# Optimization experiments

Measured on AMD Instinct MI355X. Metric: run time of the kernel, lower is better.

Reference implementation:

```python
import jax, jax.numpy as jnp
import numpy as np

D_MODEL = 1024
NUM_HEADS = 16
DEPTH = D_MODEL // NUM_HEADS  # 64
B, S = 4, 2048
NEG_BIG = -1000000000.0


def setup_inputs() -> dict:
    key = jax.random.key(0)
    ks = jax.random.split(key, 9)
    # Glorot-uniform per-head projection weights, stacked over heads: [H, d_model, depth]
    lim_qkv = np.sqrt(6.0 / (D_MODEL + DEPTH)).astype(np.float32)
    lim_o = np.sqrt(6.0 / (D_MODEL + D_MODEL)).astype(np.float32)
    x = jax.random.normal(ks[0], (B, S, D_MODEL), dtype=jnp.float32)
    attention_mask = jnp.ones((B, S, 1), dtype=jnp.float32)
    Wq = jax.random.uniform(ks[1], (NUM_HEADS, D_MODEL, DEPTH), jnp.float32, -lim_qkv, lim_qkv)
    Wk = jax.random.uniform(ks[2], (NUM_HEADS, D_MODEL, DEPTH), jnp.float32, -lim_qkv, lim_qkv)
    Wv = jax.random.uniform(ks[3], (NUM_HEADS, D_MODEL, DEPTH), jnp.float32, -lim_qkv, lim_qkv)
    bq = jnp.zeros((NUM_HEADS, DEPTH), jnp.float32)
    bk = jnp.zeros((NUM_HEADS, DEPTH), jnp.float32)
    bv = jnp.zeros((NUM_HEADS, DEPTH), jnp.float32)
    Wo = jax.random.uniform(ks[4], (D_MODEL, D_MODEL), jnp.float32, -lim_o, lim_o)
    bo = jnp.zeros((D_MODEL,), jnp.float32)
    return {"x": x, "attention_mask": attention_mask, "Wq": Wq, "bq": bq,
            "Wk": Wk, "bk": bk, "Wv": Wv, "bv": bv, "Wo": Wo, "bo": bo}


def reference(x, attention_mask, Wq, bq, Wk, bk, Wv, bv, Wo, bo):
    # Batched over heads (same math as the per-head Python loop + concat).
    # x: [B,S,D]; Wq/Wk/Wv: [H,D,depth]; bq/bk/bv: [H,depth]
    q = jnp.einsum('bsd,hde->bhse', x, Wq) + bq[None, :, None, :]
    k = jnp.einsum('bsd,hde->bhse', x, Wk) + bk[None, :, None, :]
    v = jnp.einsum('bsd,hde->bhse', x, Wv) + bv[None, :, None, :]
    scale = 1.0 / jnp.sqrt(jnp.asarray(DEPTH, dtype=x.dtype))
    scores = jnp.einsum('bhse,bhte->bhst', q, k) * scale  # [B,H,S,S]
    # original: mask.transpose(-2,-1) -> [B,1,S], broadcast over query rows; add head axis
    mask_t = jnp.swapaxes(attention_mask, -2, -1)[:, None]  # [B,1,1,S]
    scores = scores + (1.0 - mask_t) * NEG_BIG
    probs = jax.nn.softmax(scores, axis=-1)
    z = jnp.einsum('bhst,bhte->bhse', probs, v)  # [B,H,S,depth]
    # concat heads along feature dim (head order matches torch.cat order)
    multi_head = jnp.transpose(z, (0, 2, 1, 3)).reshape(x.shape[0], x.shape[1], NUM_HEADS * DEPTH)
    return multi_head @ Wo + bo
```

## Files before the change

### kernel.cpp

```cpp
#include <hip/hip_runtime.h>

#define NH 16
#define DEP 64
#define DM 1024
#define BB 4
#define SS 2048

typedef __attribute__((ext_vector_type(8))) __bf16 bf16x8;
typedef __attribute__((ext_vector_type(4))) __bf16 bf16x4;
typedef __attribute__((ext_vector_type(4))) float f32x4;
typedef unsigned short u16;

#define MFMA_BF16(A, B, C) __builtin_amdgcn_mfma_f32_16x16x32_bf16(A, B, C, 0, 0, 0)

#define SCL 0.18033688011112042f
#define LOG2E 1.4426950408889634f

__device__ __forceinline__ u16 f2bf(float f) {
  unsigned u = __builtin_bit_cast(unsigned, f);
  u += 0x7fffu + ((u >> 16) & 1u);
  return (u16)(u >> 16);
}

__device__ __forceinline__ void gload_lds16(const u16* g, u16* l) {
  __builtin_amdgcn_global_load_lds((const __attribute__((address_space(1))) void*)g,
                                   (__attribute__((address_space(3))) void*)l, 16, 0, 0);
}

__global__ __launch_bounds__(256) void k_cvt_x(const float* __restrict__ x, u16* __restrict__ xb) {
  int i = (blockIdx.x * 256 + threadIdx.x) * 4;
  float4 v = *(const float4*)(x + i);
  ushort4 o;
  o.x = f2bf(v.x); o.y = f2bf(v.y); o.z = f2bf(v.z); o.w = f2bf(v.w);
  *(ushort4*)(xb + i) = o;
}

__global__ __launch_bounds__(256) void k_pack_qkv(const float* __restrict__ Wq, const float* __restrict__ Wk,
                                                  const float* __restrict__ Wv,
                                                  const float* __restrict__ bq, const float* __restrict__ bk,
                                                  const float* __restrict__ bv,
                                                  u16* __restrict__ wt, float* __restrict__ biasN) {
  __shared__ float lt[64][65];
  int k0 = blockIdx.x * 64;
  int z = blockIdx.y;
  int which = z >> 4, h = z & 15;
  const float* W = which == 0 ? Wq : (which == 1 ? Wk : Wv);
  const float* bsrc = which == 0 ? bq : (which == 1 ? bk : bv);
  const float* src = W + (size_t)h * DM * DEP;
  int t = threadIdx.x;
#pragma unroll
  for (int p = 0; p < 16; ++p) {
    int li = p * 256 + t;
    int r = li >> 6, c = li & 63;
    lt[r][c] = src[(size_t)(k0 + r) * 64 + c];
  }
  __syncthreads();
  int woff = which * DM + h * 64;
#pragma unroll
  for (int p = 0; p < 16; ++p) {
    int li = p * 256 + t;
    int r = li >> 6, c = li & 63;
    wt[(size_t)(woff + r) * DM + k0 + c] = f2bf(lt[c][r]);
  }
  if (blockIdx.x == 0 && t < 64) biasN[woff + t] = bsrc[h * 64 + t];
}

__global__ __launch_bounds__(256) void k_pack_wo(const float* __restrict__ Wo, u16* __restrict__ wot) {
  __shared__ float lt[64][65];
  int k0 = blockIdx.x * 64, n0 = blockIdx.y * 64;
  int t = threadIdx.x;
#pragma unroll
  for (int p = 0; p < 16; ++p) {
    int li = p * 256 + t;
    int r = li >> 6, c = li & 63;
    lt[r][c] = Wo[(size_t)(k0 + r) * DM + n0 + c];
  }
  __syncthreads();
#pragma unroll
  for (int p = 0; p < 16; ++p) {
    int li = p * 256 + t;
    int r = li >> 6, c = li & 63;
    wot[(size_t)(n0 + r) * DM + k0 + c] = f2bf(lt[c][r]);
  }
}

__global__ __launch_bounds__(256) void k_maskbias(const float* __restrict__ mask, float* __restrict__ mb) {
  int i = blockIdx.x * 256 + threadIdx.x;
  mb[i] = (1.0f - mask[i]) * (-1000000000.0f * LOG2E);
}

__global__ __launch_bounds__(256) void k_gemm_qkv(const u16* __restrict__ xb, const u16* __restrict__ wt,
                                                  const float* __restrict__ biasN,
                                                  u16* __restrict__ qb, u16* __restrict__ kb,
                                                  u16* __restrict__ vtb) {
  __shared__ u16 lA[128 * 32];
  __shared__ u16 lB[128 * 32];
  const int tid = threadIdx.x;
  const int lane = tid & 63, w = tid >> 6;
  const int m0 = blockIdx.x * 128, n0 = blockIdx.y * 128;
  const int wm = (w >> 1) * 64, wn = (w & 1) * 64;
  const int fr = lane & 15, fg = lane >> 4;
  const int bidx = tid * 16;
  const int row0 = bidx >> 6, c0 = (bidx & 63) >> 1;
  f32x4 acc[4][4] = {};
  for (int k0 = 0; k0 < DM; k0 += 32) {
    __syncthreads();
    gload_lds16(xb + (size_t)(m0 + row0) * DM + k0 + c0, lA + w * 512);
    gload_lds16(xb + (size_t)(m0 + row0 + 64) * DM + k0 + c0, lA + 2048 + w * 512);
    gload_lds16(wt + (size_t)(n0 + row0) * DM + k0 + c0, lB + w * 512);
    gload_lds16(wt + (size_t)(n0 + row0 + 64) * DM + k0 + c0, lB + 2048 + w * 512);
    __syncthreads();
    bf16x8 af[4], bfr[4];
#pragma unroll
    for (int i = 0; i < 4; ++i) {
      af[i] = *(const bf16x8*)&lA[(wm + i * 16 + fr) * 32 + fg * 8];
      bfr[i] = *(const bf16x8*)&lB[(wn + i * 16 + fr) * 32 + fg * 8];
    }
#pragma unroll
    for (int i = 0; i < 4; ++i)
#pragma unroll
      for (int j = 0; j < 4; ++j)
        acc[i][j] = MFMA_BF16(af[i], bfr[j], acc[i][j]);
  }
#pragma unroll
  for (int i = 0; i < 4; ++i)
#pragma unroll
    for (int j = 0; j < 4; ++j) {
      int n = n0 + wn + j * 16 + fr;
      float bn = biasN[n];
      int which = n >> 10, rem = n & 1023, h = rem >> 6, d = rem & 63;
#pragma unroll
      for (int r = 0; r < 4; ++r) {
        int m = m0 + wm + i * 16 + fg * 4 + r;
        int b = m >> 11, s = m & 2047;
        float val = acc[i][j][r] + bn;
        if (which == 0)      qb[(((size_t)(b * NH + h) * SS + s) << 6) + d] = f2bf(val * SCL);
        else if (which == 1) kb[(((size_t)(b * NH + h) * SS + s) << 6) + d] = f2bf(val);
        else                 vtb[(((size_t)(b * NH + h) * 64 + d) << 11) + s] = f2bf(val);
      }
    }
}

__global__ __launch_bounds__(256) void k_attn(const u16* __restrict__ qb, const u16* __restrict__ kb,
                                              const u16* __restrict__ vtb, const float* __restrict__ mbias,
                                              u16* __restrict__ zb) {
  __shared__ u16 sK[2][64 * 64];
  __shared__ u16 sV[2][64 * 64];
  __shared__ u16 sP[4][32 * 64];
  const int bh = blockIdx.y;
  const int b = bh >> 4, h = bh & 15;
  const int tid = threadIdx.x, lane = tid & 63, w = tid >> 6;
  const int q0 = blockIdx.x * 128 + w * 32;
  const u16* Q  = qb  + (size_t)bh * SS * 64;
  const u16* K  = kb  + (size_t)bh * SS * 64;
  const u16* VT = vtb + (size_t)bh * 64 * SS;
  const float* mbb = mbias + b * SS;
  const int fr = lane & 15, fg = lane >> 4;
  const int fr7 = fr & 7;
  const int rsub = lane >> 3;
  const int cg = (lane & 7) ^ rsub;
  bf16x8 q0lo = *(const bf16x8*)&Q[(q0 + fr) * 64 + fg * 8];
  bf16x8 q0hi = *(const bf16x8*)&Q[(q0 + fr) * 64 + 32 + fg * 8];
  bf16x8 q1lo = *(const bf16x8*)&Q[(q0 + 16 + fr) * 64 + fg * 8];
  bf16x8 q1hi = *(const bf16x8*)&Q[(q0 + 16 + fr) * 64 + 32 + fg * 8];
  float lrun0 = 0.f, lrun1 = 0.f;
  f32x4 o0[4] = {}, o1[4] = {};

#pragma unroll
  for (int j = 0; j < 2; ++j) {
    int i = w * 2 + j;
    gload_lds16(K + (size_t)(8 * i + rsub) * 64 + cg * 8, &sK[0][i * 512]);
    gload_lds16(VT + (size_t)(8 * i + rsub) * SS + cg * 8, &sV[0][i * 512]);
  }
  __syncthreads();

  for (int t = 0; t < 32; ++t) {
    const int cur = t & 1;
    if (t < 31) {
      const int kvn = (t + 1) * 64;
#pragma unroll
      for (int j = 0; j < 2; ++j) {
        int i = w * 2 + j;
        gload_lds16(K + (size_t)(kvn + 8 * i + rsub) * 64 + cg * 8, &sK[cur ^ 1][i * 512]);
        gload_lds16(VT + (size_t)(8 * i + rsub) * SS + kvn + cg * 8, &sV[cur ^ 1][i * 512]);
      }
    }
    const int kv = t * 64;
    f32x4 sc0[4], sc1[4];
    __builtin_amdgcn_s_setprio(1);
#pragma unroll
    for (int kt = 0; kt < 4; ++kt) {
      bf16x8 klo = *(const bf16x8*)&sK[cur][(kt * 16 + fr) * 64 + ((fg ^ fr7) * 8)];
      bf16x8 khi = *(const bf16x8*)&sK[cur][(kt * 16 + fr) * 64 + (((4 + fg) ^ fr7) * 8)];
      f32x4 mb4 = *(const f32x4*)(mbb + kv + kt * 16 + fg * 4);
      sc0[kt] = MFMA_BF16(khi, q0hi, MFMA_BF16(klo, q0lo, mb4));
      sc1[kt] = MFMA_BF16(khi, q1hi, MFMA_BF16(klo, q1lo, mb4));
    }
    __builtin_amdgcn_s_setprio(0);
#pragma unroll
    for (int kt = 0; kt < 4; ++kt) {
      float a0 = __builtin_amdgcn_exp2f(sc0[kt][0]);
      float a1 = __builtin_amdgcn_exp2f(sc0[kt][1]);
      float a2 = __builtin_amdgcn_exp2f(sc0[kt][2]);
      float a3 = __builtin_amdgcn_exp2f(sc0[kt][3]);
      lrun0 += (a0 + a1) + (a2 + a3);
      bf16x4 pk0 = {(__bf16)a0, (__bf16)a1, (__bf16)a2, (__bf16)a3};
      *(bf16x4*)&sP[w][fr * 64 + (((2 * kt + (fg >> 1)) ^ fr7) * 8) + 4 * (fg & 1)] = pk0;
      float b0 = __builtin_amdgcn_exp2f(sc1[kt][0]);
      float b1 = __builtin_amdgcn_exp2f(sc1[kt][1]);
      float b2 = __builtin_amdgcn_exp2f(sc1[kt][2]);
      float b3 = __builtin_amdgcn_exp2f(sc1[kt][3]);
      lrun1 += (b0 + b1) + (b2 + b3);
      bf16x4 pk1 = {(__bf16)b0, (__bf16)b1, (__bf16)b2, (__bf16)b3};
      *(bf16x4*)&sP[w][(16 + fr) * 64 + (((2 * kt + (fg >> 1)) ^ fr7) * 8) + 4 * (fg & 1)] = pk1;
    }
    bf16x8 pa00 = *(const bf16x8*)&sP[w][fr * 64 + ((fg ^ fr7) * 8)];
    bf16x8 pa01 = *(const bf16x8*)&sP[w][fr * 64 + (((4 + fg) ^ fr7) * 8)];
    bf16x8 pa10 = *(const bf16x8*)&sP[w][(16 + fr) * 64 + ((fg ^ fr7) * 8)];
    bf16x8 pa11 = *(const bf16x8*)&sP[w][(16 + fr) * 64 + (((4 + fg) ^ fr7) * 8)];
    __builtin_amdgcn_s_setprio(1);
#pragma unroll
    for (int dc = 0; dc < 4; ++dc) {
      bf16x8 v0 = *(const bf16x8*)&sV[cur][(dc * 16 + fr) * 64 + ((fg ^ fr7) * 8)];
      bf16x8 v1 = *(const bf16x8*)&sV[cur][(dc * 16 + fr) * 64 + (((4 + fg) ^ fr7) * 8)];
      o0[dc] = MFMA_BF16(pa00, v0, o0[dc]);
      o0[dc] = MFMA_BF16(pa01, v1, o0[dc]);
      o1[dc] = MFMA_BF16(pa10, v0, o1[dc]);
      o1[dc] = MFMA_BF16(pa11, v1, o1[dc]);
    }
    __builtin_amdgcn_s_setprio(0);
    __syncthreads();
  }
  float l0 = lrun0; l0 += __shfl_xor(l0, 16); l0 += __shfl_xor(l0, 32);
  float l1 = lrun1; l1 += __shfl_xor(l1, 16); l1 += __shfl_xor(l1, 32);
#pragma unroll
  for (int r = 0; r < 4; ++r) {
    float i0 = 1.0f / __shfl(l0, 4 * fg + r);
    float i1 = 1.0f / __shfl(l1, 4 * fg + r);
    int s0 = q0 + 4 * fg + r, s1 = q0 + 16 + 4 * fg + r;
#pragma unroll
    for (int dc = 0; dc < 4; ++dc) {
      zb[(size_t)(b * SS + s0) * DM + h * 64 + dc * 16 + fr] = f2bf(o0[dc][r] * i0);
      zb[(size_t)(b * SS + s1) * DM + h * 64 + dc * 16 + fr] = f2bf(o1[dc][r] * i1);
    }
  }
}

__global__ __launch_bounds__(256) void k_gemm_out(const u16* __restrict__ zb, const u16* __restrict__ wot,
                                                  const float* __restrict__ bo, float* __restrict__ out) {
  __shared__ u16 lA[128 * 32];
  __shared__ u16 lB[128 * 32];
  const int tid = threadIdx.x;
  const int lane = tid & 63, w = tid >> 6;
  const int m0 = blockIdx.x * 128, n0 = blockIdx.y * 128;
  const int wm = (w >> 1) * 64, wn = (w & 1) * 64;
  const int fr = lane & 15, fg = lane >> 4;
  const int bidx = tid * 16;
  const int row0 = bidx >> 6, c0 = (bidx & 63) >> 1;
  f32x4 acc[4][4] = {};
  for (int k0 = 0; k0 < DM; k0 += 32) {
    __syncthreads();
    gload_lds16(zb + (size_t)(m0 + row0) * DM + k0 + c0, lA + w * 512);
    gload_lds16(zb + (size_t)(m0 + row0 + 64) * DM + k0 + c0, lA + 2048 + w * 512);
    gload_lds16(wot + (size_t)(n0 + row0) * DM + k0 + c0, lB + w * 512);
    gload_lds16(wot + (size_t)(n0 + row0 + 64) * DM + k0 + c0, lB + 2048 + w * 512);
    __syncthreads();
    bf16x8 af[4], bfr[4];
#pragma unroll
    for (int i = 0; i < 4; ++i) {
      af[i] = *(const bf16x8*)&lA[(wm + i * 16 + fr) * 32 + fg * 8];
      bfr[i] = *(const bf16x8*)&lB[(wn + i * 16 + fr) * 32 + fg * 8];
    }
#pragma unroll
    for (int i = 0; i < 4; ++i)
#pragma unroll
      for (int j = 0; j < 4; ++j)
        acc[i][j] = MFMA_BF16(af[i], bfr[j], acc[i][j]);
  }
#pragma unroll
  for (int i = 0; i < 4; ++i)
#pragma unroll
    for (int j = 0; j < 4; ++j) {
      int n = n0 + wn + j * 16 + fr;
      float bn = bo[n];
#pragma unroll
      for (int r = 0; r < 4; ++r) {
        int m = m0 + wm + i * 16 + fg * 4 + r;
        out[(size_t)m * DM + n] = acc[i][j][r] + bn;
      }
    }
}

extern "C" void kernel_launch(void* const* d_in, const int* in_sizes, int n_in,
                              void* d_out, int out_size, void* d_ws, size_t ws_size,
                              hipStream_t stream) {
  const float* x    = (const float*)d_in[0];
  const float* mask = (const float*)d_in[1];
  const float* Wq   = (const float*)d_in[2];
  const float* bq   = (const float*)d_in[3];
  const float* Wk   = (const float*)d_in[4];
  const float* bk   = (const float*)d_in[5];
  const float* Wv   = (const float*)d_in[6];
  const float* bv   = (const float*)d_in[7];
  const float* Wo   = (const float*)d_in[8];
  const float* bo   = (const float*)d_in[9];
  char* ws = (char*)d_ws;
  u16*   xb    = (u16*)(ws + 0);
  u16*   zb    = xb;
  u16*   wt    = (u16*)(ws + 16777216);
  u16*   wot   = (u16*)(ws + 23068672);
  float* biasN = (float*)(ws + 25165824);
  float* mb    = (float*)(ws + 25178112);
  u16*   qb    = (u16*)(ws + 25210880);
  u16*   kb    = (u16*)(ws + 41988096);
  u16*   vtb   = (u16*)(ws + 58765312);
  float* out   = (float*)d_out;

  k_cvt_x<<<dim3(8192), dim3(256), 0, stream>>>(x, xb);
  k_pack_qkv<<<dim3(16, 48), dim3(256), 0, stream>>>(Wq, Wk, Wv, bq, bk, bv, wt, biasN);
  k_pack_wo<<<dim3(16, 16), dim3(256), 0, stream>>>(Wo, wot);
  k_maskbias<<<dim3(32), dim3(256), 0, stream>>>(mask, mb);
  k_gemm_qkv<<<dim3(64, 24), dim3(256), 0, stream>>>(xb, wt, biasN, qb, kb, vtb);
  k_attn<<<dim3(16, 64), dim3(256), 0, stream>>>(qb, kb, vtb, mb, zb);
  k_gemm_out<<<dim3(64, 8), dim3(256), 0, stream>>>(zb, wot, bo, out);
}
```

Measured before the change: 243.1 us.

## Keep attention probabilities in registers and enlarge per-wave query tile to 64

The attention kernel no longer stages softmax probabilities through LDS. Instead, it packs exp values into bf16 pairs and uses cross-lane shuffles to build the MFMA A operand directly, with V fragments loaded in a permuted order to match. Each wave now handles 64 query rows instead of 32, so K/V LDS fragments are reused across four query fragments, and the grid is halved. This cuts LDS traffic and barriers per key tile. In exchange it raises register pressure (launch bounds set to 2 blocks) and reduces the number of blocks.

```diff
diff --git a/kernel.cpp b/kernel.cpp
--- a/kernel.cpp
+++ b/kernel.cpp
@@ -8,7 +8,10 @@
 
 typedef __attribute__((ext_vector_type(8))) __bf16 bf16x8;
 typedef __attribute__((ext_vector_type(4))) __bf16 bf16x4;
+typedef __attribute__((ext_vector_type(2))) __bf16 bf16x2;
 typedef __attribute__((ext_vector_type(4))) float f32x4;
+typedef __attribute__((ext_vector_type(4))) unsigned u32x4;
+typedef __attribute__((ext_vector_type(2))) unsigned u32x2;
 typedef unsigned short u16;
 
 #define MFMA_BF16(A, B, C) __builtin_amdgcn_mfma_f32_16x16x32_bf16(A, B, C, 0, 0, 0)
@@ -20,6 +23,12 @@
   unsigned u = __builtin_bit_cast(unsigned, f);
   u += 0x7fffu + ((u >> 16) & 1u);
   return (u16)(u >> 16);
+}
+
+__device__ __forceinline__ unsigned pk2(float a, float b) {
+  bf16x2 t;
+  t[0] = (__bf16)a; t[1] = (__bf16)b;
+  return __builtin_bit_cast(unsigned, t);
 }
 
 __device__ __forceinline__ void gload_lds16(const u16* g, u16* l) {
@@ -141,16 +150,15 @@
     }
 }
 
-__global__ __launch_bounds__(256) void k_attn(const u16* __restrict__ qb, const u16* __restrict__ kb,
-                                              const u16* __restrict__ vtb, const float* __restrict__ mbias,
-                                              u16* __restrict__ zb) {
+__global__ __launch_bounds__(256, 2) void k_attn(const u16* __restrict__ qb, const u16* __restrict__ kb,
+                                                 const u16* __restrict__ vtb, const float* __restrict__ mbias,
+                                                 u16* __restrict__ zb) {
   __shared__ u16 sK[2][64 * 64];
   __shared__ u16 sV[2][64 * 64];
-  __shared__ u16 sP[4][32 * 64];
   const int bh = blockIdx.y;
   const int b = bh >> 4, h = bh & 15;
   const int tid = threadIdx.x, lane = tid & 63, w = tid >> 6;
-  const int q0 = blockIdx.x * 128 + w * 32;
+  const int q0 = blockIdx.x * 256 + w * 64;
   const u16* Q  = qb  + (size_t)bh * SS * 64;
   const u16* K  = kb  + (size_t)bh * SS * 64;
   const u16* VT = vtb + (size_t)bh * 64 * SS;
@@ -159,12 +167,21 @@
   const int fr7 = fr & 7;
   const int rsub = lane >> 3;
   const int cg = (lane & 7) ^ rsub;
-  bf16x8 q0lo = *(const bf16x8*)&Q[(q0 + fr) * 64 + fg * 8];
-  bf16x8 q0hi = *(const bf16x8*)&Q[(q0 + fr) * 64 + 32 + fg * 8];
-  bf16x8 q1lo = *(const bf16x8*)&Q[(q0 + 16 + fr) * 64 + fg * 8];
-  bf16x8 q1hi = *(const bf16x8*)&Q[(q0 + 16 + fr) * 64 + 32 + fg * 8];
-  float lrun0 = 0.f, lrun1 = 0.f;
-  f32x4 o0[4] = {}, o1[4] = {};
+  const int kc0 = (fg ^ fr7) * 16;
+  const int kc1 = ((4 + fg) ^ fr7) * 16;
+  const int fg1 = fg >> 1, fgb = (fg & 1) * 8;
+  const int cX0 = (((fg1)     ^ fr7)) * 16 + fgb;
+  const int cX1 = (((2 + (fg1 ^ 1)) ^ fr7)) * 16 + fgb;
+  const int cY0 = (((4 + fg1) ^ fr7)) * 16 + fgb;
+  const int cY1 = (((6 + (fg1 ^ 1)) ^ fr7)) * 16 + fgb;
+  bf16x8 qlo[4], qhi[4];
+#pragma unroll
+  for (int qf = 0; qf < 4; ++qf) {
+    qlo[qf] = *(const bf16x8*)&Q[(q0 + 16 * qf + fr) * 64 + fg * 8];
+    qhi[qf] = *(const bf16x8*)&Q[(q0 + 16 * qf + fr) * 64 + 32 + fg * 8];
+  }
+  float lrun[4] = {0.f, 0.f, 0.f, 0.f};
+  f32x4 o[4][4] = {};
 
 #pragma unroll
   for (int j = 0; j < 2; ++j) {
@@ -186,62 +203,81 @@
       }
     }
     const int kv = t * 64;
-    f32x4 sc0[4], sc1[4];
-    __builtin_amdgcn_s_setprio(1);
+    const char* Kb = (const char*)&sK[cur][0];
+    const char* Vb = (const char*)&sV[cur][0];
+    bf16x8 klo[4], khi[4];
 #pragma unroll
     for (int kt = 0; kt < 4; ++kt) {
-      bf16x8 klo = *(const bf16x8*)&sK[cur][(kt * 16 + fr) * 64 + ((fg ^ fr7) * 8)];
-      bf16x8 khi = *(const bf16x8*)&sK[cur][(kt * 16 + fr) * 64 + (((4 + fg) ^ fr7) * 8)];
-      f32x4 mb4 = *(const f32x4*)(mbb + kv + kt * 16 + fg * 4);
-      sc0[kt] = MFMA_BF16(khi, q0hi, MFMA_BF16(klo, q0lo, mb4));
-      sc1[kt] = MFMA_BF16(khi, q1hi, MFMA_BF16(klo, q1lo, mb4));
-    }
-    __builtin_amdgcn_s_setprio(0);
-#pragma unroll
-    for (int kt = 0; kt < 4; ++kt) {
-      float a0 = __builtin_amdgcn_exp2f(sc0[kt][0]);
-      float a1 = __builtin_amdgcn_exp2f(sc0[kt][1]);
-      float a2 = __builtin_amdgcn_exp2f(sc0[kt][2]);
-      float a3 = __builtin_amdgcn_exp2f(sc0[kt][3]);
-      lrun0 += (a0 + a1) + (a2 + a3);
-      bf16x4 pk0 = {(__bf16)a0, (__bf16)a1, (__bf16)a2, (__bf16)a3};
-      *(bf16x4*)&sP[w][fr * 64 + (((2 * kt + (fg >> 1)) ^ fr7) * 8) + 4 * (fg & 1)] = pk0;
-      float b0 = __builtin_amdgcn_exp2f(sc1[kt][0]);
-      float b1 = __builtin_amdgcn_exp2f(sc1[kt][1]);
-      float b2 = __builtin_amdgcn_exp2f(sc1[kt][2]);
-      float b3 = __builtin_amdgcn_exp2f(sc1[kt][3]);
-      lrun1 += (b0 + b1) + (b2 + b3);
-      bf16x4 pk1 = {(__bf16)b0, (__bf16)b1, (__bf16)b2, (__bf16)b3};
-      *(bf16x4*)&sP[w][(16 + fr) * 64 + (((2 * kt + (fg >> 1)) ^ fr7) * 8) + 4 * (fg & 1)] = pk1;
-    }
-    bf16x8 pa00 = *(const bf16x8*)&sP[w][fr * 64 + ((fg ^ fr7) * 8)];
-    bf16x8 pa01 = *(const bf16x8*)&sP[w][fr * 64 + (((4 + fg) ^ fr7) * 8)];
-    bf16x8 pa10 = *(const bf16x8*)&sP[w][(16 + fr) * 64 + ((fg ^ fr7) * 8)];
-    bf16x8 pa11 = *(const bf16x8*)&sP[w][(16 + fr) * 64 + (((4 + fg) ^ fr7) * 8)];
-    __builtin_amdgcn_s_setprio(1);
+      klo[kt] = *(const bf16x8*)(Kb + (kt * 16 + fr) * 128 + kc0);
+      khi[kt] = *(const bf16x8*)(Kb + (kt * 16 + fr) * 128 + kc1);
+    }
+    u32x2 vx0[4], vx1[4], vy0[4], vy1[4];
 #pragma unroll
     for (int dc = 0; dc < 4; ++dc) {
-      bf16x8 v0 = *(const bf16x8*)&sV[cur][(dc * 16 + fr) * 64 + ((fg ^ fr7) * 8)];
-      bf16x8 v1 = *(const bf16x8*)&sV[cur][(dc * 16 + fr) * 64 + (((4 + fg) ^ fr7) * 8)];
-      o0[dc] = MFMA_BF16(pa00, v0, o0[dc]);
-      o0[dc] = MFMA_BF16(pa01, v1, o0[dc]);
-      o1[dc] = MFMA_BF16(pa10, v0, o1[dc]);
-      o1[dc] = MFMA_BF16(pa11, v1, o1[dc]);
-    }
-    __builtin_amdgcn_s_setprio(0);
-    __syncthreads();
-  }
-  float l0 = lrun0; l0 += __shfl_xor(l0, 16); l0 += __shfl_xor(l0, 32);
-  float l1 = lrun1; l1 += __shfl_xor(l1, 16); l1 += __shfl_xor(l1, 32);
-#pragma unroll
-  for (int r = 0; r < 4; ++r) {
-    float i0 = 1.0f / __shfl(l0, 4 * fg + r);
-    float i1 = 1.0f / __shfl(l1, 4 * fg + r);
-    int s0 = q0 + 4 * fg + r, s1 = q0 + 16 + 4 * fg + r;
-#pragma unroll
-    for (int dc = 0; dc < 4; ++dc) {
-      zb[(size_t)(b * SS + s0) * DM + h * 64 + dc * 16 + fr] = f2bf(o0[dc][r] * i0);
-      zb[(size_t)(b * SS + s1) * DM + h * 64 + dc * 16 + fr] = f2bf(o1[dc][r] * i1);
+      const char* rb = Vb + (dc * 16 + fr) * 128;
+      vx0[dc] = *(const u32x2*)(rb + cX0);
+      vx1[dc] = *(const u32x2*)(rb + cX1);
+      vy0[dc] = *(const u32x2*)(rb + cY0);
+      vy1[dc] = *(const u32x2*)(rb + cY1);
+    }
+#pragma unroll
+    for (int qf = 0; qf < 4; ++qf) {
+      f32x4 sc[4];
+      __builtin_amdgcn_s_setprio(1);
+#pragma unroll
+      for (int kt = 0; kt < 4; ++kt) {
+        f32x4 mb4 = *(const f32x4*)(mbb + kv + kt * 16 + fg * 4);
+        sc[kt] = MFMA_BF16(khi[kt], qhi[qf], MFMA_BF16(klo[kt], qlo[qf], mb4));
+      }
+      __builtin_amdgcn_s_setprio(0);
+      float e00 = __builtin_amdgcn_exp2f(sc[0][0]), e01 = __builtin_amdgcn_exp2f(sc[0][1]);
+      float e02 = __builtin_amdgcn_exp2f(sc[0][2]), e03 = __builtin_amdgcn_exp2f(sc[0][3]);
+      float e10 = __builtin_amdgcn_exp2f(sc[1][0]), e11 = __builtin_amdgcn_exp2f(sc[1][1]);
+      float e12 = __builtin_amdgcn_exp2f(sc[1][2]), e13 = __builtin_amdgcn_exp2f(sc[1][3]);
+      float e20 = __builtin_amdgcn_exp2f(sc[2][0]), e21 = __builtin_amdgcn_exp2f(sc[2][1]);
+      float e22 = __builtin_amdgcn_exp2f(sc[2][2]), e23 = __builtin_amdgcn_exp2f(sc[2][3]);
+      float e30 = __builtin_amdgcn_exp2f(sc[3][0]), e31 = __builtin_amdgcn_exp2f(sc[3][1]);
+      float e32 = __builtin_amdgcn_exp2f(sc[3][2]), e33 = __builtin_amdgcn_exp2f(sc[3][3]);
+      lrun[qf] += ((e00 + e01) + (e02 + e03)) + ((e10 + e11) + (e12 + e13))
+                + ((e20 + e21) + (e22 + e23)) + ((e30 + e31) + (e32 + e33));
+      unsigned w00 = pk2(e00, e01), w01 = pk2(e02, e03);
+      unsigned w10 = pk2(e10, e11), w11 = pk2(e12, e13);
+      unsigned w20 = pk2(e20, e21), w21 = pk2(e22, e23);
+      unsigned w30 = pk2(e30, e31), w31 = pk2(e32, e33);
+      unsigned x2 = (unsigned)__shfl_xor((int)w10, 32);
+      unsigned x3 = (unsigned)__shfl_xor((int)w11, 32);
+      unsigned y2 = (unsigned)__shfl_xor((int)w30, 32);
+      unsigned y3 = (unsigned)__shfl_xor((int)w31, 32);
+      u32x4 ux = {w00, w01, x2, x3};
+      u32x4 uy = {w20, w21, y2, y3};
+      bf16x8 paX = __builtin_bit_cast(bf16x8, ux);
+      bf16x8 paY = __builtin_bit_cast(bf16x8, uy);
+      __builtin_amdgcn_s_setprio(1);
+#pragma unroll
+      for (int dc = 0; dc < 4; ++dc) {
+        u32x4 vxw = {vx0[dc][0], vx0[dc][1], vx1[dc][0], vx1[dc][1]};
+        u32x4 vyw = {vy0[dc][0], vy0[dc][1], vy1[dc][0], vy1[dc][1]};
+        bf16x8 vX = __builtin_bit_cast(bf16x8, vxw);
+        bf16x8 vY = __builtin_bit_cast(bf16x8, vyw);
+        o[qf][dc] = MFMA_BF16(paX, vX, o[qf][dc]);
+        o[qf][dc] = MFMA_BF16(paY, vY, o[qf][dc]);
+      }
+      __builtin_amdgcn_s_setprio(0);
+    }
+    __syncthreads();
+  }
+#pragma unroll
+  for (int qf = 0; qf < 4; ++qf) {
+    float l = lrun[qf];
+    l += __shfl_xor(l, 16);
+    l += __shfl_xor(l, 32);
+#pragma unroll
+    for (int r = 0; r < 4; ++r) {
+      float linv = 1.0f / __shfl(l, 4 * fg + r);
+      int s = q0 + 16 * qf + 4 * fg + r;
+#pragma unroll
+      for (int dc = 0; dc < 4; ++dc)
+        zb[(size_t)(b * SS + s) * DM + h * 64 + dc * 16 + fr] = f2bf(o[qf][dc][r] * linv);
     }
   }
 }
@@ -321,6 +357,6 @@
   k_pack_wo<<<dim3(16, 16), dim3(256), 0, stream>>>(Wo, wot);
   k_maskbias<<<dim3(32), dim3(256), 0, stream>>>(mask, mb);
   k_gemm_qkv<<<dim3(64, 24), dim3(256), 0, stream>>>(xb, wt, biasN, qb, kb, vtb);
-  k_attn<<<dim3(16, 64), dim3(256), 0, stream>>>(qb, kb, vtb, mb, zb);
+  k_attn<<<dim3(8, 64), dim3(256), 0, stream>>>(qb, kb, vtb, mb, zb);
   k_gemm_out<<<dim3(64, 8), dim3(256), 0, stream>>>(zb, wot, bo, out);
 }
```

Result: faster. 219.7 us (-9.6%).
